# Performance work log

Measured on AMD Instinct MI355X. Metric: run time of the kernel, lower is better.

## Reference

```python
import jax, jax.numpy as jnp
import numpy as np

BSZ, SEQ, DK = 16, 2048, 64


def setup_inputs() -> dict:
    key = jax.random.key(0)
    kq, kk, kv, kp = jax.random.split(key, 4)
    Q = jax.random.normal(kq, (BSZ, SEQ, DK), dtype=jnp.float32)
    K = jax.random.normal(kk, (BSZ, SEQ, DK), dtype=jnp.float32)
    V = jax.random.normal(kv, (BSZ, SEQ, DK), dtype=jnp.float32)
    # learned relative-position key projection, Parameter(dk, sizeSeq)
    Krelpos = jax.random.normal(kp, (DK, SEQ), dtype=jnp.float32) * (1.0 / np.sqrt(DK))
    return {"Q": Q, "K": K, "V": V, "Krelpos": Krelpos}


def reference(Q, K, V, Krelpos):
    b, S, dk = Q.shape
    # content scores: [b, S, S]
    QK = jnp.einsum('bsd,btd->bst', Q, K)
    # relative-position bias via skew trick
    QP = jnp.einsum('bsd,dt->bst', Q, Krelpos)                     # [b, S, S]
    QP = jnp.concatenate([jnp.zeros((b, S, 1), QP.dtype), QP], axis=2)  # [b, S, S+1]
    QK = QK + QP.reshape(b, S + 1, S)[:, 1:, :]                    # skewed -> [b, S, S]
    # causal mask: -inf strictly above diagonal
    causal = jnp.tril(jnp.ones((S, S), dtype=bool))
    mask = jnp.where(causal, jnp.zeros((), QK.dtype), -jnp.inf)
    A = jax.nn.softmax(QK / jnp.sqrt(jnp.asarray(dk, QK.dtype)) + mask, axis=2)
    # dropout p=0.0 -> identity
    return jnp.einsum('bst,btd->bsd', A, V)
```

## Files before the change

kernel.cpp:

```cpp
#include <hip/hip_runtime.h>
#include <math.h>

#define BSZ 16
#define SEQ 2048
#define DKD 64
#define NTH 256

typedef __attribute__((ext_vector_type(8))) short bf16x8;
typedef __attribute__((ext_vector_type(8))) short short8;
typedef __attribute__((ext_vector_type(4))) float f32x4;

__device__ __forceinline__ short f2bf(float x) {
  union { float f; unsigned u; } c; c.f = x;
  unsigned r = c.u + 0x7fffu + ((c.u >> 16) & 1u);
  return (short)(r >> 16);
}

__device__ __forceinline__ int pkbf(float hi, float lo) {
  return (int)__builtin_amdgcn_perm(__float_as_uint(hi), __float_as_uint(lo), 0x07060302u);
}

#define GLD16(gsrc, ldst)                                                                  \
  __builtin_amdgcn_global_load_lds((const __attribute__((address_space(1))) void*)(gsrc), \
                                   (__attribute__((address_space(3))) void*)(ldst), 16, 0, 0)

#define CH(row, c8) (((row) << 3) + ((c8) ^ ((row) & 7)))


__launch_bounds__(NTH)
__global__ void pre_convert(const float* __restrict__ K, const float* __restrict__ V,
                            const float* __restrict__ P, short* __restrict__ Kbf,
                            short* __restrict__ VTbf, short* __restrict__ PTbf,
                            float* __restrict__ Ozero, float* __restrict__ Lzero) {
  __shared__ short T[64 * 65];
  const int blk = blockIdx.x;
  const int tid = threadIdx.x;
  if (blk < 1024) {
    const int b = blk >> 6, ch = blk & 63;
    const float* Kb = K + ((size_t)(b * SEQ + ch * 32)) * DKD;
    const float* Vb = V + ((size_t)(b * SEQ + ch * 32)) * DKD;
    const int r = tid >> 3, c8 = (tid & 7) << 3;
    float4 a0 = *(const float4*)(Kb + r * DKD + c8);
    float4 a1 = *(const float4*)(Kb + r * DKD + c8 + 4);
    short8 ko;
    ko[0] = f2bf(a0.x); ko[1] = f2bf(a0.y); ko[2] = f2bf(a0.z); ko[3] = f2bf(a0.w);
    ko[4] = f2bf(a1.x); ko[5] = f2bf(a1.y); ko[6] = f2bf(a1.z); ko[7] = f2bf(a1.w);
    *(short8*)(Kbf + ((size_t)(b * SEQ + ch * 32 + r)) * DKD + c8) = ko;
    float4 v0 = *(const float4*)(Vb + r * DKD + c8);
    float4 v1 = *(const float4*)(Vb + r * DKD + c8 + 4);
    T[(c8 + 0) * 33 + r] = f2bf(v0.x); T[(c8 + 1) * 33 + r] = f2bf(v0.y);
    T[(c8 + 2) * 33 + r] = f2bf(v0.z); T[(c8 + 3) * 33 + r] = f2bf(v0.w);
    T[(c8 + 4) * 33 + r] = f2bf(v1.x); T[(c8 + 5) * 33 + r] = f2bf(v1.y);
    T[(c8 + 6) * 33 + r] = f2bf(v1.z); T[(c8 + 7) * 33 + r] = f2bf(v1.w);
    __syncthreads();
    const int d = tid >> 2, qg = tid & 3;
    short8 w;
    #pragma unroll
    for (int j = 0; j < 4; ++j) {
      w[j]     = T[d * 33 + qg * 4 + j];
      w[4 + j] = T[d * 33 + 16 + qg * 4 + j];
    }
    *(short8*)(VTbf + ((size_t)(b * DKD + d)) * SEQ + ch * 32 + qg * 8) = w;
  } else if (blk < 1056) {
    const int c0 = (blk - 1024) * 64;
    const int d = tid >> 2, cc4 = (tid & 3) << 4;
    #pragma unroll
    for (int j4 = 0; j4 < 4; ++j4) {
      const int c = cc4 + j4 * 4;
      float4 pv = *(const float4*)(P + (size_t)d * SEQ + c0 + c);
      T[(c + 0) * 65 + d] = f2bf(pv.x);
      T[(c + 1) * 65 + d] = f2bf(pv.y);
      T[(c + 2) * 65 + d] = f2bf(pv.z);
      T[(c + 3) * 65 + d] = f2bf(pv.w);
    }
    __syncthreads();
    const int c = tid >> 2, d4 = (tid & 3) << 4;
    short8 w0, w1;
    #pragma unroll
    for (int j = 0; j < 8; ++j) { w0[j] = T[c * 65 + d4 + j]; w1[j] = T[c * 65 + d4 + 8 + j]; }
    short* Po = PTbf + ((size_t)(c0 + c)) * DKD + d4;
    *(short8*)(Po + 0) = w0;
    *(short8*)(Po + 8) = w1;
  } else if (blk == 1056) {
    short8 z = {0, 0, 0, 0, 0, 0, 0, 0};
    short* Po = PTbf + (size_t)SEQ * DKD + tid * 16;
    *(short8*)(Po + 0) = z;
    *(short8*)(Po + 8) = z;
  } else if (blk < 1569) {
    const int u = blk - 1057;
    float4 z = {0.f, 0.f, 0.f, 0.f};
    float4* p = (float4*)(Ozero + (size_t)u * 4096 + tid * 16);
    p[0] = z; p[1] = z; p[2] = z; p[3] = z;
  } else {
    const int u = blk - 1569;
    float4 z = {0.f, 0.f, 0.f, 0.f};
    float4* p = (float4*)(Lzero + (size_t)u * 4096 + tid * 16);
    p[0] = z; p[1] = z; p[2] = z; p[3] = z;
  }
}

__launch_bounds__(NTH, 4)
__global__ void attn_split(const float* __restrict__ Q,
                           const short* __restrict__ Kbf,
                           const short* __restrict__ VTbf,
                           const short* __restrict__ PTbf,
                           float* __restrict__ Oacc,
                           float* __restrict__ Lacc) {
  __shared__ __align__(16) short smem[16384];
  short* Ks  = smem;
  short* VsT = smem + 4096;
  short* PsT = smem + 8192;

  const int tid = threadIdx.x;
  const int lane = tid & 63;
  const int wave = tid >> 6;
  const int l16 = lane & 15;
  const int quad = lane >> 4;

  const int i = blockIdx.x;
  const int qidx = i >> 6;
  const int s = i & 63;
  const int b = s >> 2;
  const int h = s & 3;
  const int qt = (qidx < 16) ? (31 - qidx) : (qidx - 16);
  const int r0 = qt * 64;
  const int kt0 = ((qt + 1) * h) >> 2;
  const int kt1 = ((qt + 1) * (h + 1)) >> 2;
  const float SC = 0.125f * 1.4426950408889634f;

  bf16x8 aq[2];
  {
    const float* Qr = Q + ((size_t)(b * SEQ + r0 + wave * 16 + l16)) * DKD + quad * 8;
    #pragma unroll
    for (int ks = 0; ks < 2; ++ks) {
      float4 x = *(const float4*)(Qr + ks * 32);
      float4 y = *(const float4*)(Qr + ks * 32 + 4);
      bf16x8 t;
      t[0] = f2bf(x.x * SC); t[1] = f2bf(x.y * SC); t[2] = f2bf(x.z * SC); t[3] = f2bf(x.w * SC);
      t[4] = f2bf(y.x * SC); t[5] = f2bf(y.y * SC); t[6] = f2bf(y.z * SC); t[7] = f2bf(y.w * SC);
      aq[ks] = t;
    }
  }

  int gsrc[4];
  bool gcar[4];
  #pragma unroll
  for (int r = 0; r < 4; ++r) {
    int o = 15 - (quad * 4 + r);
    int ss = l16 + o;
    gsrc[r] = (quad << 4) | (ss & 15);
    gcar[r] = (ss >= 16);
  }

  union i4v { int4 i; bf16x8 v; };
  i4v ONESu; ONESu.i = make_int4(0x3F803F80, 0x3F803F80, 0x3F803F80, 0x3F803F80);
  i4v S0u, S1u;
  S0u.i = make_int4(0, 0, 0, 0);
  S1u.i = make_int4(0, 0, 0, 0);
  if (quad == (l16 >> 2)) {
    const int j = l16 & 3;
    const int val = 0x3F80 << ((j & 1) * 16);
    if (j < 2) { S0u.i.x = val; S1u.i.z = val; }
    else       { S0u.i.y = val; S1u.i.w = val; }
  }

  f32x4 oacc[4];
  #pragma unroll
  for (int t = 0; t < 4; ++t)
    #pragma unroll
    for (int j = 0; j < 4; ++j) oacc[t][j] = 0.f;
  f32x4 bl;
  #pragma unroll
  for (int j = 0; j < 4; ++j) bl[j] = 0.f;

  const int Blo0 = 31 - qt;

  for (int kt = kt0; kt < kt1; ++kt) {
    const int j0 = kt * 64;
    __syncthreads();

    #pragma unroll
    for (int half = 0; half < 2; ++half) {
      const int ii = wave * 2 + half;
      const int j = ii * 64 + lane;
      {
        const int k = j >> 3, c8 = (j & 7) ^ (k & 7);
        GLD16(Kbf + ((size_t)(b * SEQ + j0 + k)) * DKD + c8 * 8, Ks + ii * 512);
      }
      {
        const int d = j >> 3, c8 = (j & 7) ^ (d & 7);
        GLD16(VTbf + ((size_t)(b * DKD + d)) * SEQ + j0 + c8 * 8, VsT + ii * 512);
      }
    }
    {
      const int Bg = Blo0 + kt + 1;
      #pragma unroll
      for (int half = 0; half < 2; ++half) {
        const int ii = wave * 2 + half;
        const int j = ii * 64 + lane;
        const int c = j >> 3, c8 = (j & 7) ^ (c & 7);
        GLD16(PTbf + ((size_t)(Bg * 64 + c)) * DKD + c8 * 8,
              PsT + ((Bg & 1) << 12) + ii * 512);
      }
      if (kt == kt0) {
        const int Bl = Blo0 + kt0;
        #pragma unroll
        for (int half = 0; half < 2; ++half) {
          const int ii = wave * 2 + half;
          const int j = ii * 64 + lane;
          const int c = j >> 3, c8 = (j & 7) ^ (c & 7);
          GLD16(PTbf + ((size_t)(Bl * 64 + c)) * DKD + c8 * 8,
                PsT + ((Bl & 1) << 12) + ii * 512);
        }
      }
    }
    __syncthreads();

    f32x4 sacc[4];
    #pragma unroll
    for (int t = 0; t < 4; ++t)
      #pragma unroll
      for (int j = 0; j < 4; ++j) sacc[t][j] = 0.f;
    #pragma unroll
    for (int ks = 0; ks < 2; ++ks)
      #pragma unroll
      for (int t = 0; t < 4; ++t) {
        bf16x8 bk = *(const bf16x8*)&Ks[CH(t * 16 + l16, ks * 4 + quad) << 3];
        sacc[t] = __builtin_amdgcn_mfma_f32_16x16x32_bf16(aq[ks], bk, sacc[t], 0, 0, 0);
      }

    float g[5][4];
    #pragma unroll
    for (int tt = 0; tt < 5; ++tt) {
      f32x4 bacc;
      #pragma unroll
      for (int j = 0; j < 4; ++j) bacc[j] = 0.f;
      const int c = (tt + 3 - wave) * 16 + l16;
      const int pan = (Blo0 + kt + (c >> 6)) & 1;
      const int pr = c & 63;
      #pragma unroll
      for (int ks = 0; ks < 2; ++ks) {
        bf16x8 bp = *(const bf16x8*)&PsT[(pan << 12) + (CH(pr, ks * 4 + quad) << 3)];
        bacc = __builtin_amdgcn_mfma_f32_16x16x32_bf16(aq[ks], bp, bacc, 0, 0, 0);
      }
      #pragma unroll
      for (int r = 0; r < 4; ++r) g[tt][r] = __shfl(bacc[r], gsrc[r], 64);
    }

    const bool diag = (kt == qt);
    float e[4][4];
    #pragma unroll
    for (int t = 0; t < 4; ++t)
      #pragma unroll
      for (int r = 0; r < 4; ++r) {
        float sc = sacc[t][r] + (gcar[r] ? g[t + 1][r] : g[t][r]);
        if (diag && (t * 16 + l16 > wave * 16 + quad * 4 + r)) sc = -INFINITY;
        e[t][r] = exp2f(sc);
      }

    i4v ap0, ap1;
    ap0.i.x = pkbf(e[0][1], e[0][0]); ap0.i.y = pkbf(e[0][3], e[0][2]);
    ap0.i.z = pkbf(e[1][1], e[1][0]); ap0.i.w = pkbf(e[1][3], e[1][2]);
    ap1.i.x = pkbf(e[2][1], e[2][0]); ap1.i.y = pkbf(e[2][3], e[2][2]);
    ap1.i.z = pkbf(e[3][1], e[3][0]); ap1.i.w = pkbf(e[3][3], e[3][2]);

    f32x4 zero4;
    #pragma unroll
    for (int j = 0; j < 4; ++j) zero4[j] = 0.f;
    f32x4 Dt[4];
    Dt[0] = __builtin_amdgcn_mfma_f32_16x16x32_bf16(ap0.v, S0u.v, zero4, 0, 0, 0);
    Dt[1] = __builtin_amdgcn_mfma_f32_16x16x32_bf16(ap0.v, S1u.v, zero4, 0, 0, 0);
    Dt[2] = __builtin_amdgcn_mfma_f32_16x16x32_bf16(ap1.v, S0u.v, zero4, 0, 0, 0);
    Dt[3] = __builtin_amdgcn_mfma_f32_16x16x32_bf16(ap1.v, S1u.v, zero4, 0, 0, 0);

    i4v bp0, bp1;
    bp0.i.x = pkbf(Dt[0][1], Dt[0][0]); bp0.i.y = pkbf(Dt[0][3], Dt[0][2]);
    bp0.i.z = pkbf(Dt[1][1], Dt[1][0]); bp0.i.w = pkbf(Dt[1][3], Dt[1][2]);
    bp1.i.x = pkbf(Dt[2][1], Dt[2][0]); bp1.i.y = pkbf(Dt[2][3], Dt[2][2]);
    bp1.i.z = pkbf(Dt[3][1], Dt[3][0]); bp1.i.w = pkbf(Dt[3][3], Dt[3][2]);

    #pragma unroll
    for (int tp = 0; tp < 2; ++tp) {
      const bf16x8 bpk = tp ? bp1.v : bp0.v;
      bl = __builtin_amdgcn_mfma_f32_16x16x32_bf16(ONESu.v, bpk, bl, 0, 0, 0);
      #pragma unroll
      for (int dt = 0; dt < 4; ++dt) {
        bf16x8 av = *(const bf16x8*)&VsT[CH(dt * 16 + l16, tp * 4 + quad) << 3];
        oacc[dt] = __builtin_amdgcn_mfma_f32_16x16x32_bf16(av, bpk, oacc[dt], 0, 0, 0);
      }
    }
  }

  __syncthreads();
  float* Te = (float*)smem;
  #pragma unroll
  for (int dt = 0; dt < 4; ++dt)
    #pragma unroll
    for (int r = 0; r < 4; ++r)
      Te[(wave * 16 + l16) * 65 + dt * 16 + quad * 4 + r] = oacc[dt][r];
  __syncthreads();
  if (kt1 > kt0) {
    float* Ob = Oacc + ((size_t)(b * SEQ + r0)) * DKD;
    #pragma unroll
    for (int j = 0; j < 16; ++j) {
      const int idx = j * NTH + tid;
      const int row = idx >> 6, col = idx & 63;
      unsafeAtomicAdd(&Ob[(size_t)row * DKD + col], Te[row * 65 + col]);
    }
    if (quad == 0)
      unsafeAtomicAdd(&Lacc[b * SEQ + r0 + wave * 16 + l16], bl[0]);
  }
}

__launch_bounds__(NTH)
__global__ void norm_out(float* __restrict__ O, const float* __restrict__ L) {
  const int tid = threadIdx.x;
  const int row = blockIdx.x * 16 + (tid >> 4);
  const int c4 = (tid & 15) << 2;
  const float rl = 1.0f / L[row];
  float4* p = (float4*)(O + (size_t)row * DKD + c4);
  float4 v = *p;
  v.x *= rl; v.y *= rl; v.z *= rl; v.w *= rl;
  *p = v;
}

extern "C" void kernel_launch(void* const* d_in, const int* in_sizes, int n_in,
                              void* d_out, int out_size, void* d_ws, size_t ws_size,
                              hipStream_t stream) {
  const float* Q = (const float*)d_in[0];
  const float* K = (const float*)d_in[1];
  const float* V = (const float*)d_in[2];
  const float* P = (const float*)d_in[3];
  float* O = (float*)d_out;

  short* Kbf = (short*)d_ws;
  short* VTbf = (short*)((char*)d_ws + 4194304);
  short* PTbf = (short*)((char*)d_ws + 8388608);
  float* Lacc = (float*)((char*)d_ws + 8658944);

  hipLaunchKernelGGL(pre_convert, dim3(1577), dim3(NTH), 0, stream,
                     K, V, P, Kbf, VTbf, PTbf, O, Lacc);
  hipLaunchKernelGGL(attn_split, dim3(2048), dim3(NTH), 0, stream,
                     Q, Kbf, VTbf, PTbf, O, Lacc);
  hipLaunchKernelGGL(norm_out, dim3(BSZ * SEQ / 16), dim3(NTH), 0, stream, O, Lacc);
}
```

Before: 128.9 us.

## Double query tile to 128 rows per block to reuse K/V/P tiles

Each block now processes 128 query rows instead of 64. Each wave handles two 16-row subtiles, so every K, V and relative-position tile loaded into LDS feeds twice as many MFMAs. The relative-position panel buffer grows to a 3-slot ring and the padding region of PTbf is extended, with matching workspace offset and grid changes. The intent is to halve global/LDS traffic per FLOP and the number of atomic output flushes. In exchange it uses more registers and LDS, which may lower occupancy, and the grid halves to 1024 blocks.

```diff
diff --git a/kernel.cpp b/kernel.cpp
--- a/kernel.cpp
+++ b/kernel.cpp
@@ -81,18 +81,18 @@
     short* Po = PTbf + ((size_t)(c0 + c)) * DKD + d4;
     *(short8*)(Po + 0) = w0;
     *(short8*)(Po + 8) = w1;
-  } else if (blk == 1056) {
+  } else if (blk < 1058) {
     short8 z = {0, 0, 0, 0, 0, 0, 0, 0};
-    short* Po = PTbf + (size_t)SEQ * DKD + tid * 16;
+    short* Po = PTbf + ((size_t)SEQ + (blk - 1056) * 64) * DKD + tid * 16;
     *(short8*)(Po + 0) = z;
     *(short8*)(Po + 8) = z;
-  } else if (blk < 1569) {
-    const int u = blk - 1057;
+  } else if (blk < 1570) {
+    const int u = blk - 1058;
     float4 z = {0.f, 0.f, 0.f, 0.f};
     float4* p = (float4*)(Ozero + (size_t)u * 4096 + tid * 16);
     p[0] = z; p[1] = z; p[2] = z; p[3] = z;
   } else {
-    const int u = blk - 1569;
+    const int u = blk - 1570;
     float4 z = {0.f, 0.f, 0.f, 0.f};
     float4* p = (float4*)(Lzero + (size_t)u * 4096 + tid * 16);
     p[0] = z; p[1] = z; p[2] = z; p[3] = z;
@@ -106,7 +106,7 @@
                            const short* __restrict__ PTbf,
                            float* __restrict__ Oacc,
                            float* __restrict__ Lacc) {
-  __shared__ __align__(16) short smem[16384];
+  __shared__ __align__(16) short smem[20480];
   short* Ks  = smem;
   short* VsT = smem + 4096;
   short* PsT = smem + 8192;
@@ -122,15 +122,17 @@
   const int s = i & 63;
   const int b = s >> 2;
   const int h = s & 3;
-  const int qt = (qidx < 16) ? (31 - qidx) : (qidx - 16);
-  const int r0 = qt * 64;
-  const int kt0 = ((qt + 1) * h) >> 2;
-  const int kt1 = ((qt + 1) * (h + 1)) >> 2;
+  const int qt = (qidx < 8) ? (15 - qidx) : (qidx - 8);
+  const int r0 = qt * 128;
+  const int nk = 2 * qt + 2;
+  const int kt0 = (nk * h) >> 2;
+  const int kt1 = (nk * (h + 1)) >> 2;
   const float SC = 0.125f * 1.4426950408889634f;
 
-  bf16x8 aq[2];
-  {
-    const float* Qr = Q + ((size_t)(b * SEQ + r0 + wave * 16 + l16)) * DKD + quad * 8;
+  bf16x8 aq[2][2];
+  #pragma unroll
+  for (int st = 0; st < 2; ++st) {
+    const float* Qr = Q + ((size_t)(b * SEQ + r0 + wave * 32 + st * 16 + l16)) * DKD + quad * 8;
     #pragma unroll
     for (int ks = 0; ks < 2; ++ks) {
       float4 x = *(const float4*)(Qr + ks * 32);
@@ -138,7 +140,7 @@
       bf16x8 t;
       t[0] = f2bf(x.x * SC); t[1] = f2bf(x.y * SC); t[2] = f2bf(x.z * SC); t[3] = f2bf(x.w * SC);
       t[4] = f2bf(y.x * SC); t[5] = f2bf(y.y * SC); t[6] = f2bf(y.z * SC); t[7] = f2bf(y.w * SC);
-      aq[ks] = t;
+      aq[st][ks] = t;
     }
   }
 
@@ -164,19 +166,23 @@
     else       { S0u.i.y = val; S1u.i.w = val; }
   }
 
-  f32x4 oacc[4];
-  #pragma unroll
-  for (int t = 0; t < 4; ++t)
-    #pragma unroll
-    for (int j = 0; j < 4; ++j) oacc[t][j] = 0.f;
-  f32x4 bl;
-  #pragma unroll
-  for (int j = 0; j < 4; ++j) bl[j] = 0.f;
-
-  const int Blo0 = 31 - qt;
+  f32x4 oacc[2][4];
+  #pragma unroll
+  for (int st = 0; st < 2; ++st)
+    #pragma unroll
+    for (int t = 0; t < 4; ++t)
+      #pragma unroll
+      for (int j = 0; j < 4; ++j) oacc[st][t][j] = 0.f;
+  f32x4 bl[2];
+  #pragma unroll
+  for (int st = 0; st < 2; ++st)
+    #pragma unroll
+    for (int j = 0; j < 4; ++j) bl[st][j] = 0.f;
 
   for (int kt = kt0; kt < kt1; ++kt) {
     const int j0 = kt * 64;
+    const int PL = 30 - 2 * qt + kt;
+    const int PLmod = PL % 3;
     __syncthreads();
 
     #pragma unroll
@@ -193,100 +199,108 @@
       }
     }
     {
-      const int Bg = Blo0 + kt + 1;
+      const int ii = wave * 2;
       #pragma unroll
       for (int half = 0; half < 2; ++half) {
-        const int ii = wave * 2 + half;
-        const int j = ii * 64 + lane;
+        const int j = (ii + half) * 64 + lane;
         const int c = j >> 3, c8 = (j & 7) ^ (c & 7);
-        GLD16(PTbf + ((size_t)(Bg * 64 + c)) * DKD + c8 * 8,
-              PsT + ((Bg & 1) << 12) + ii * 512);
-      }
-      if (kt == kt0) {
-        const int Bl = Blo0 + kt0;
-        #pragma unroll
-        for (int half = 0; half < 2; ++half) {
-          const int ii = wave * 2 + half;
-          const int j = ii * 64 + lane;
-          const int c = j >> 3, c8 = (j & 7) ^ (c & 7);
-          GLD16(PTbf + ((size_t)(Bl * 64 + c)) * DKD + c8 * 8,
-                PsT + ((Bl & 1) << 12) + ii * 512);
+        {
+          const int Pg = PL + 2;
+          GLD16(PTbf + ((size_t)(Pg * 64 + c)) * DKD + c8 * 8,
+                PsT + (Pg % 3) * 4096 + (ii + half) * 512);
         }
+        if (kt == kt0) {
+          GLD16(PTbf + ((size_t)(PL * 64 + c)) * DKD + c8 * 8,
+                PsT + PLmod * 4096 + (ii + half) * 512);
+          const int P1 = PL + 1;
+          GLD16(PTbf + ((size_t)(P1 * 64 + c)) * DKD + c8 * 8,
+                PsT + (P1 % 3) * 4096 + (ii + half) * 512);
+        }
       }
     }
     __syncthreads();
 
-    f32x4 sacc[4];
-    #pragma unroll
-    for (int t = 0; t < 4; ++t)
-      #pragma unroll
-      for (int j = 0; j < 4; ++j) sacc[t][j] = 0.f;
+    f32x4 sacc[2][4];
+    #pragma unroll
+    for (int st = 0; st < 2; ++st)
+      #pragma unroll
+      for (int t = 0; t < 4; ++t)
+        #pragma unroll
+        for (int j = 0; j < 4; ++j) sacc[st][t][j] = 0.f;
     #pragma unroll
     for (int ks = 0; ks < 2; ++ks)
       #pragma unroll
       for (int t = 0; t < 4; ++t) {
         bf16x8 bk = *(const bf16x8*)&Ks[CH(t * 16 + l16, ks * 4 + quad) << 3];
-        sacc[t] = __builtin_amdgcn_mfma_f32_16x16x32_bf16(aq[ks], bk, sacc[t], 0, 0, 0);
-      }
-
-    float g[5][4];
-    #pragma unroll
-    for (int tt = 0; tt < 5; ++tt) {
-      f32x4 bacc;
-      #pragma unroll
-      for (int j = 0; j < 4; ++j) bacc[j] = 0.f;
-      const int c = (tt + 3 - wave) * 16 + l16;
-      const int pan = (Blo0 + kt + (c >> 6)) & 1;
-      const int pr = c & 63;
-      #pragma unroll
-      for (int ks = 0; ks < 2; ++ks) {
-        bf16x8 bp = *(const bf16x8*)&PsT[(pan << 12) + (CH(pr, ks * 4 + quad) << 3)];
-        bacc = __builtin_amdgcn_mfma_f32_16x16x32_bf16(aq[ks], bp, bacc, 0, 0, 0);
-      }
-      #pragma unroll
-      for (int r = 0; r < 4; ++r) g[tt][r] = __shfl(bacc[r], gsrc[r], 64);
-    }
-
-    const bool diag = (kt == qt);
-    float e[4][4];
-    #pragma unroll
-    for (int t = 0; t < 4; ++t)
-      #pragma unroll
-      for (int r = 0; r < 4; ++r) {
-        float sc = sacc[t][r] + (gcar[r] ? g[t + 1][r] : g[t][r]);
-        if (diag && (t * 16 + l16 > wave * 16 + quad * 4 + r)) sc = -INFINITY;
-        e[t][r] = exp2f(sc);
-      }
-
-    i4v ap0, ap1;
-    ap0.i.x = pkbf(e[0][1], e[0][0]); ap0.i.y = pkbf(e[0][3], e[0][2]);
-    ap0.i.z = pkbf(e[1][1], e[1][0]); ap0.i.w = pkbf(e[1][3], e[1][2]);
-    ap1.i.x = pkbf(e[2][1], e[2][0]); ap1.i.y = pkbf(e[2][3], e[2][2]);
-    ap1.i.z = pkbf(e[3][1], e[3][0]); ap1.i.w = pkbf(e[3][3], e[3][2]);
-
-    f32x4 zero4;
-    #pragma unroll
-    for (int j = 0; j < 4; ++j) zero4[j] = 0.f;
-    f32x4 Dt[4];
-    Dt[0] = __builtin_amdgcn_mfma_f32_16x16x32_bf16(ap0.v, S0u.v, zero4, 0, 0, 0);
-    Dt[1] = __builtin_amdgcn_mfma_f32_16x16x32_bf16(ap0.v, S1u.v, zero4, 0, 0, 0);
-    Dt[2] = __builtin_amdgcn_mfma_f32_16x16x32_bf16(ap1.v, S0u.v, zero4, 0, 0, 0);
-    Dt[3] = __builtin_amdgcn_mfma_f32_16x16x32_bf16(ap1.v, S1u.v, zero4, 0, 0, 0);
-
-    i4v bp0, bp1;
-    bp0.i.x = pkbf(Dt[0][1], Dt[0][0]); bp0.i.y = pkbf(Dt[0][3], Dt[0][2]);
-    bp0.i.z = pkbf(Dt[1][1], Dt[1][0]); bp0.i.w = pkbf(Dt[1][3], Dt[1][2]);
-    bp1.i.x = pkbf(Dt[2][1], Dt[2][0]); bp1.i.y = pkbf(Dt[2][3], Dt[2][2]);
-    bp1.i.z = pkbf(Dt[3][1], Dt[3][0]); bp1.i.w = pkbf(Dt[3][3], Dt[3][2]);
+        sacc[0][t] = __builtin_amdgcn_mfma_f32_16x16x32_bf16(aq[0][ks], bk, sacc[0][t], 0, 0, 0);
+        sacc[1][t] = __builtin_amdgcn_mfma_f32_16x16x32_bf16(aq[1][ks], bk, sacc[1][t], 0, 0, 0);
+      }
+
+    i4v bpk[2][2];
+    #pragma unroll
+    for (int st = 0; st < 2; ++st) {
+      const int T0 = 7 - 2 * wave - st;
+      const int dj = j0 - (r0 + wave * 32 + st * 16);
+      float g[5][4];
+      #pragma unroll
+      for (int tt = 0; tt < 5; ++tt) {
+        f32x4 bacc;
+        #pragma unroll
+        for (int j = 0; j < 4; ++j) bacc[j] = 0.f;
+        const int T = T0 + tt;
+        int sl = PLmod + (T >> 2);
+        sl = (sl >= 3) ? sl - 3 : sl;
+        const int pc = ((T & 3) << 4) + l16;
+        #pragma unroll
+        for (int ks = 0; ks < 2; ++ks) {
+          bf16x8 bp = *(const bf16x8*)&PsT[sl * 4096 + (CH(pc, ks * 4 + quad) << 3)];
+          bacc = __builtin_amdgcn_mfma_f32_16x16x32_bf16(aq[st][ks], bp, bacc, 0, 0, 0);
+        }
+        #pragma unroll
+        for (int r = 0; r < 4; ++r) g[tt][r] = __shfl(bacc[r], gsrc[r], 64);
+      }
+
+      const bool dg = (dj > -63);
+      float e[4][4];
+      #pragma unroll
+      for (int t = 0; t < 4; ++t)
+        #pragma unroll
+        for (int r = 0; r < 4; ++r) {
+          float sc = sacc[st][t][r] + (gcar[r] ? g[t + 1][r] : g[t][r]);
+          if (dg && (dj + t * 16 + l16 > quad * 4 + r)) sc = -INFINITY;
+          e[t][r] = exp2f(sc);
+        }
+
+      i4v ap0, ap1;
+      ap0.i.x = pkbf(e[0][1], e[0][0]); ap0.i.y = pkbf(e[0][3], e[0][2]);
+      ap0.i.z = pkbf(e[1][1], e[1][0]); ap0.i.w = pkbf(e[1][3], e[1][2]);
+      ap1.i.x = pkbf(e[2][1], e[2][0]); ap1.i.y = pkbf(e[2][3], e[2][2]);
+      ap1.i.z = pkbf(e[3][1], e[3][0]); ap1.i.w = pkbf(e[3][3], e[3][2]);
+
+      f32x4 zero4;
+      #pragma unroll
+      for (int j = 0; j < 4; ++j) zero4[j] = 0.f;
+      f32x4 Dt[4];
+      Dt[0] = __builtin_amdgcn_mfma_f32_16x16x32_bf16(ap0.v, S0u.v, zero4, 0, 0, 0);
+      Dt[1] = __builtin_amdgcn_mfma_f32_16x16x32_bf16(ap0.v, S1u.v, zero4, 0, 0, 0);
+      Dt[2] = __builtin_amdgcn_mfma_f32_16x16x32_bf16(ap1.v, S0u.v, zero4, 0, 0, 0);
+      Dt[3] = __builtin_amdgcn_mfma_f32_16x16x32_bf16(ap1.v, S1u.v, zero4, 0, 0, 0);
+
+      bpk[st][0].i.x = pkbf(Dt[0][1], Dt[0][0]); bpk[st][0].i.y = pkbf(Dt[0][3], Dt[0][2]);
+      bpk[st][0].i.z = pkbf(Dt[1][1], Dt[1][0]); bpk[st][0].i.w = pkbf(Dt[1][3], Dt[1][2]);
+      bpk[st][1].i.x = pkbf(Dt[2][1], Dt[2][0]); bpk[st][1].i.y = pkbf(Dt[2][3], Dt[2][2]);
+      bpk[st][1].i.z = pkbf(Dt[3][1], Dt[3][0]); bpk[st][1].i.w = pkbf(Dt[3][3], Dt[3][2]);
+    }
 
     #pragma unroll
     for (int tp = 0; tp < 2; ++tp) {
-      const bf16x8 bpk = tp ? bp1.v : bp0.v;
-      bl = __builtin_amdgcn_mfma_f32_16x16x32_bf16(ONESu.v, bpk, bl, 0, 0, 0);
+      bl[0] = __builtin_amdgcn_mfma_f32_16x16x32_bf16(ONESu.v, bpk[0][tp].v, bl[0], 0, 0, 0);
+      bl[1] = __builtin_amdgcn_mfma_f32_16x16x32_bf16(ONESu.v, bpk[1][tp].v, bl[1], 0, 0, 0);
       #pragma unroll
       for (int dt = 0; dt < 4; ++dt) {
         bf16x8 av = *(const bf16x8*)&VsT[CH(dt * 16 + l16, tp * 4 + quad) << 3];
-        oacc[dt] = __builtin_amdgcn_mfma_f32_16x16x32_bf16(av, bpk, oacc[dt], 0, 0, 0);
+        oacc[0][dt] = __builtin_amdgcn_mfma_f32_16x16x32_bf16(av, bpk[0][tp].v, oacc[0][dt], 0, 0, 0);
+        oacc[1][dt] = __builtin_amdgcn_mfma_f32_16x16x32_bf16(av, bpk[1][tp].v, oacc[1][dt], 0, 0, 0);
       }
     }
   }
@@ -294,21 +308,26 @@
   __syncthreads();
   float* Te = (float*)smem;
   #pragma unroll
-  for (int dt = 0; dt < 4; ++dt)
-    #pragma unroll
-    for (int r = 0; r < 4; ++r)
-      Te[(wave * 16 + l16) * 65 + dt * 16 + quad * 4 + r] = oacc[dt][r];
+  for (int st = 0; st < 2; ++st)
+    #pragma unroll
+    for (int dt = 0; dt < 4; ++dt)
+      #pragma unroll
+      for (int r = 0; r < 4; ++r)
+        Te[(wave * 32 + st * 16 + l16) * 65 + dt * 16 + quad * 4 + r] = oacc[st][dt][r];
   __syncthreads();
   if (kt1 > kt0) {
     float* Ob = Oacc + ((size_t)(b * SEQ + r0)) * DKD;
     #pragma unroll
-    for (int j = 0; j < 16; ++j) {
+    for (int j = 0; j < 32; ++j) {
       const int idx = j * NTH + tid;
       const int row = idx >> 6, col = idx & 63;
       unsafeAtomicAdd(&Ob[(size_t)row * DKD + col], Te[row * 65 + col]);
     }
-    if (quad == 0)
-      unsafeAtomicAdd(&Lacc[b * SEQ + r0 + wave * 16 + l16], bl[0]);
+    if (quad == 0) {
+      #pragma unroll
+      for (int st = 0; st < 2; ++st)
+        unsafeAtomicAdd(&Lacc[b * SEQ + r0 + wave * 32 + st * 16 + l16], bl[st][0]);
+    }
   }
 }
 
@@ -336,11 +355,11 @@
   short* Kbf = (short*)d_ws;
   short* VTbf = (short*)((char*)d_ws + 4194304);
   short* PTbf = (short*)((char*)d_ws + 8388608);
-  float* Lacc = (float*)((char*)d_ws + 8658944);
-
-  hipLaunchKernelGGL(pre_convert, dim3(1577), dim3(NTH), 0, stream,
+  float* Lacc = (float*)((char*)d_ws + 8667136);
+
+  hipLaunchKernelGGL(pre_convert, dim3(1578), dim3(NTH), 0, stream,
                      K, V, P, Kbf, VTbf, PTbf, O, Lacc);
-  hipLaunchKernelGGL(attn_split, dim3(2048), dim3(NTH), 0, stream,
+  hipLaunchKernelGGL(attn_split, dim3(1024), dim3(NTH), 0, stream,
                      Q, Kbf, VTbf, PTbf, O, Lacc);
   hipLaunchKernelGGL(norm_out, dim3(BSZ * SEQ / 16), dim3(NTH), 0, stream, O, Lacc);
 }
```

After: 178.4 us. 38.4% more time.
